# Kernel optimization log

Hardware: AMD Instinct MI355X
Metric: run time of the kernel (lower is better)

## Reference

```python
import jax, jax.numpy as jnp
import numpy as np

N, E, D, H, O, G = 50000, 640000, 128, 128, 16, 64


def setup_inputs() -> dict:
    key = jax.random.key(0)
    ks = jax.random.split(key, 10)
    x = jax.random.normal(ks[0], (N, D), dtype=jnp.float32)
    edge_index = jax.random.randint(ks[1], (2, E), 0, N, dtype=jnp.int64)
    edge_weight = jax.random.uniform(ks[2], (E,), dtype=jnp.float32)
    batch = jnp.sort(jax.random.randint(ks[3], (N,), 0, G, dtype=jnp.int64))
    s1 = 1.0 / np.sqrt(D)
    s2 = 1.0 / np.sqrt(H)
    W1 = jax.random.uniform(ks[4], (D, H), jnp.float32, -s1, s1)
    b1 = jnp.zeros((H,), jnp.float32)
    W2 = jax.random.uniform(ks[5], (H, H), jnp.float32, -s2, s2)
    b2 = jnp.zeros((H,), jnp.float32)
    Wfc = jax.random.uniform(ks[6], (H, O), jnp.float32, -s2, s2)
    bfc = jax.random.uniform(ks[7], (O,), jnp.float32, -s2, s2)
    return dict(x=x, edge_index=edge_index, edge_weight=edge_weight, batch=batch,
                W1=W1, b1=b1, W2=W2, b2=b2, Wfc=Wfc, bfc=bfc)


def _gcn_conv(x, row, col, ew, W, b, n):
    # PyG GCNConv: out[i] = sum_{(j->i)} norm_ji * (x[j] @ W) + b
    xw = x @ W
    deg = jax.ops.segment_sum(ew, col, num_segments=n)          # [N]
    dinv = jnp.where(deg > 0, jax.lax.rsqrt(deg), 0.0)
    norm = dinv[row] * ew * dinv[col]                           # [E+N]
    msg = xw[row] * norm[:, None]                               # gather + scale
    return jax.ops.segment_sum(msg, col, num_segments=n) + b    # scatter-add


def reference(x, edge_index, edge_weight, batch, W1, b1, W2, b2, Wfc, bfc):
    n = x.shape[0]
    # add self-loops with weight 1 (PyG gcn_norm default)
    loop = jnp.arange(n, dtype=edge_index.dtype)
    row = jnp.concatenate([edge_index[0], loop])
    col = jnp.concatenate([edge_index[1], loop])
    ew = jnp.concatenate([edge_weight, jnp.ones((n,), edge_weight.dtype)])

    h = jax.nn.relu(_gcn_conv(x, row, col, ew, W1, b1, n))
    h = jax.nn.relu(_gcn_conv(h, row, col, ew, W2, b2, n))

    # global_mean_pool over graph ids
    sums = jax.ops.segment_sum(h, batch, num_segments=G)        # [G, H]
    cnt = jax.ops.segment_sum(jnp.ones((n,), h.dtype), batch, num_segments=G)
    pooled = sums / jnp.maximum(cnt, 1.0)[:, None]
    return pooled @ Wfc + bfc                                   # [G, O]
```

## Files before the change

kernel.cpp:

```cpp
#include <hip/hip_runtime.h>


typedef _Float16 h4 __attribute__((ext_vector_type(4)));
typedef _Float16 h8 __attribute__((ext_vector_type(8)));
typedef float f32x4 __attribute__((ext_vector_type(4)));

__global__ void initcnt_kernel(int* __restrict__ cnt, int NC) {
    int i = blockIdx.x * blockDim.x + threadIdx.x;
    if (i < NC) cnt[i] = 0;
}

__global__ void rank_kernel(const int* __restrict__ row, const int* __restrict__ col,
                            int* __restrict__ cnt, int* __restrict__ rank, int E, int C) {
    int e = blockIdx.x * blockDim.x + threadIdx.x;
    if (e >= E) return;
    int key = col[e] * C + (row[e] >> 13);
    rank[e] = atomicAdd(&cnt[key], 1);
}

__global__ void block_sum_kernel(const int* __restrict__ cnt, int* __restrict__ bsum, int NC) {
    __shared__ int s[512];
    int t = threadIdx.x;
    int i = blockIdx.x * 512 + t;
    s[t] = (i < NC) ? cnt[i] : 0;
    __syncthreads();
    for (int off = 256; off > 0; off >>= 1) {
        if (t < off) s[t] += s[t + off];
        __syncthreads();
    }
    if (t == 0) bsum[blockIdx.x] = s[0];
}

__global__ void scan_bsum_kernel(const int* __restrict__ bsum, int* __restrict__ boff,
                                 int* __restrict__ rowptr, int NC, int nb) {
    __shared__ int s[1024];
    int t = threadIdx.x;
    int v = (t < nb) ? bsum[t] : 0;
    s[t] = v;
    __syncthreads();
    for (int off = 1; off < 1024; off <<= 1) {
        int u = (t >= off) ? s[t - off] : 0;
        __syncthreads();
        s[t] += u;
        __syncthreads();
    }
    if (t < nb) boff[t] = s[t] - v;
    if (t == nb - 1) rowptr[NC] = s[t];
}

__global__ void rowptr_kernel(const int* __restrict__ cnt, const int* __restrict__ boff,
                              int* __restrict__ rowptr, int NC) {
    __shared__ int s[512];
    int t = threadIdx.x;
    int i = blockIdx.x * 512 + t;
    int v = (i < NC) ? cnt[i] : 0;
    s[t] = v;
    __syncthreads();
    for (int off = 1; off < 512; off <<= 1) {
        int u = (t >= off) ? s[t - off] : 0;
        __syncthreads();
        s[t] += u;
        __syncthreads();
    }
    if (i < NC) rowptr[i] = boff[blockIdx.x] + s[t] - v;
}

__global__ void scatter_kernel(const int* __restrict__ row, const int* __restrict__ col,
                               const float* __restrict__ ew, const int* __restrict__ rank,
                               const int* __restrict__ rowptr, int2* __restrict__ csr,
                               int E, int C) {
    int e = blockIdx.x * blockDim.x + threadIdx.x;
    if (e >= E) return;
    int r = row[e];
    int pos = rowptr[col[e] * C + (r >> 13)] + rank[e];
    int2 v;
    v.x = r;
    v.y = __float_as_int(ew[e]);
    csr[pos] = v;
}

__global__ __launch_bounds__(256) void deginv_convert_kernel(
        const float4* __restrict__ x4, const int2* __restrict__ csr,
        const int* __restrict__ rowptr, float* __restrict__ dinv,
        h4* __restrict__ p16, int n, int C) {
    int node = blockIdx.x * 8 + (threadIdx.x >> 5);
    if (node >= n) return;
    int lane = threadIdx.x & 31;
    int beg = rowptr[node * C], end = rowptr[node * C + C];
    float sum = 0.0f;
    for (int k = beg + lane; k < end; k += 32) sum += __int_as_float(csr[k].y);
#pragma unroll
    for (int m = 16; m >= 1; m >>= 1) sum += __shfl_xor(sum, m);
    float di = rsqrtf(1.0f + sum);
    if (lane == 0) dinv[node] = di;
    float4 v = x4[(size_t)node * 32 + lane];
    h4 h;
    h.x = (_Float16)(di * v.x); h.y = (_Float16)(di * v.y);
    h.z = (_Float16)(di * v.z); h.w = (_Float16)(di * v.w);
    p16[(size_t)node * 32 + lane] = h;
}

__global__ __launch_bounds__(256) void agg_kernel(const h4* __restrict__ in16,
                                                  const int* __restrict__ rowptr,
                                                  const int2* __restrict__ csr,
                                                  const float* __restrict__ dinv,
                                                  h4* __restrict__ out16, int n, int C) {
    int node = blockIdx.x * 8 + (threadIdx.x >> 5);
    if (node >= n) return;
    int lane = threadIdx.x & 31;
    float di = dinv[node];
    h4 v = in16[(size_t)node * 32 + lane];
    float ax = (float)v.x, ay = (float)v.y, az = (float)v.z, aw = (float)v.w;
    int beg = rowptr[node * C], end = rowptr[node * C + C];
    int idx = beg;
    for (; idx + 4 <= end; idx += 4) {
        int2 e0 = csr[idx + 0], e1 = csr[idx + 1], e2 = csr[idx + 2], e3 = csr[idx + 3];
        h4 u0 = in16[(size_t)e0.x * 32 + lane];
        h4 u1 = in16[(size_t)e1.x * 32 + lane];
        h4 u2 = in16[(size_t)e2.x * 32 + lane];
        h4 u3 = in16[(size_t)e3.x * 32 + lane];
        float w0 = __int_as_float(e0.y), w1 = __int_as_float(e1.y);
        float w2 = __int_as_float(e2.y), w3 = __int_as_float(e3.y);
        ax += w0 * (float)u0.x; ay += w0 * (float)u0.y; az += w0 * (float)u0.z; aw += w0 * (float)u0.w;
        ax += w1 * (float)u1.x; ay += w1 * (float)u1.y; az += w1 * (float)u1.z; aw += w1 * (float)u1.w;
        ax += w2 * (float)u2.x; ay += w2 * (float)u2.y; az += w2 * (float)u2.z; aw += w2 * (float)u2.w;
        ax += w3 * (float)u3.x; ay += w3 * (float)u3.y; az += w3 * (float)u3.z; aw += w3 * (float)u3.w;
    }
    for (; idx < end; ++idx) {
        int2 e0 = csr[idx];
        float ww = __int_as_float(e0.y);
        h4 u = in16[(size_t)e0.x * 32 + lane];
        ax += ww * (float)u.x; ay += ww * (float)u.y;
        az += ww * (float)u.z; aw += ww * (float)u.w;
    }
    h4 r;
    r.x = (_Float16)(ax * di); r.y = (_Float16)(ay * di);
    r.z = (_Float16)(az * di); r.w = (_Float16)(aw * di);
    out16[(size_t)node * 32 + lane] = r;
}

__global__ __launch_bounds__(256) void packW_kernel(const float* __restrict__ W1,
                                                    const float* __restrict__ W2,
                                                    _Float16* __restrict__ Wp1,
                                                    _Float16* __restrict__ Wp2) {
    const float* W = blockIdx.x ? W2 : W1;
    _Float16* Wp = blockIdx.x ? Wp2 : Wp1;
    for (int i = threadIdx.x; i < 2048; i += 256) {
        int lane = i & 63, kc = i >> 6;
        int c = kc >> 2, kb = kc & 3;
        int colq = lane & 15, quad = lane >> 4;
        h8 v;
#pragma unroll
        for (int j = 0; j < 8; ++j)
            v[j] = (_Float16)W[(kb * 32 + quad * 8 + j) * 128 + c * 16 + colq];
        ((h8*)Wp)[i] = v;
    }
}

template <int SCALE>
__global__ __launch_bounds__(256) void gemm_mfma(const _Float16* __restrict__ A,
                                                 const h8* __restrict__ Wp,
                                                 const float* __restrict__ bias,
                                                 const float* __restrict__ dinv,
                                                 _Float16* __restrict__ out16, int n) {
    int wid = threadIdx.x >> 6, lane = threadIdx.x & 63;
    int tb = blockIdx.x * 64 + wid * 16;
    if (tb >= n) return;
    int colq = lane & 15, quad = lane >> 4;

    int arow = tb + colq;
    if (arow >= n) arow = n - 1;
    const h8* Arow = (const h8*)(A + (size_t)arow * 128);
    h8 a[4];
#pragma unroll
    for (int kb = 0; kb < 4; ++kb) a[kb] = Arow[kb * 4 + quad];

    f32x4 acc[8];
#pragma unroll
    for (int c = 0; c < 8; ++c) acc[c] = (f32x4)(0.0f);

#pragma unroll
    for (int c = 0; c < 8; ++c) {
#pragma unroll
        for (int kb = 0; kb < 4; ++kb) {
            h8 b = Wp[(c * 4 + kb) * 64 + lane];
            acc[c] = __builtin_amdgcn_mfma_f32_16x16x32_f16(a[kb], b, acc[c], 0, 0, 0);
        }
    }

#pragma unroll
    for (int c = 0; c < 8; ++c) {
        float bz = bias[c * 16 + colq];
#pragma unroll
        for (int r = 0; r < 4; ++r) {
            int row = tb + quad * 4 + r;
            if (row < n) {
                float v = fmaxf(acc[c][r] + bz, 0.0f);
                if (SCALE) v *= dinv[row];
                out16[(size_t)row * 128 + c * 16 + colq] = (_Float16)v;
            }
        }
    }
}

__global__ __launch_bounds__(256) void poolfc_kernel(const h4* __restrict__ h,
                                                     const int* __restrict__ batch,
                                                     const float* __restrict__ Wfc,
                                                     const float* __restrict__ bfc,
                                                     float* __restrict__ out, int n, int O) {
    int g = blockIdx.x;
    __shared__ int sb[2];
    __shared__ float4 red[256];
    __shared__ float pooled[128];
    int t = threadIdx.x;
    if (t < 2) {
        int target = g + t;
        int lo = 0, hi = n;
        while (lo < hi) { int m = (lo + hi) >> 1; if (batch[m] < target) lo = m + 1; else hi = m; }
        sb[t] = lo;
    }
    __syncthreads();
    int start = sb[0], end = sb[1], len = end - start;
    int gq = t & 31;
    int seg = t >> 5;
    float4 acc; acc.x = acc.y = acc.z = acc.w = 0.0f;
    for (int i = start + seg; i < end; i += 8) {
        h4 v = h[(size_t)i * 32 + gq];
        acc.x += (float)v.x; acc.y += (float)v.y;
        acc.z += (float)v.z; acc.w += (float)v.w;
    }
    red[seg * 32 + gq] = acc;
    __syncthreads();
    if (t < 128) {
        float4 a = red[t], b = red[t + 128];
        a.x += b.x; a.y += b.y; a.z += b.z; a.w += b.w;
        red[t] = a;
    }
    __syncthreads();
    if (t < 64) {
        float4 a = red[t], b = red[t + 64];
        a.x += b.x; a.y += b.y; a.z += b.z; a.w += b.w;
        red[t] = a;
    }
    __syncthreads();
    if (t < 32) {
        float4 a = red[t], b = red[t + 32];
        float inv = (len > 0) ? 1.0f / (float)len : 0.0f;
        pooled[t * 4 + 0] = (a.x + b.x) * inv;
        pooled[t * 4 + 1] = (a.y + b.y) * inv;
        pooled[t * 4 + 2] = (a.z + b.z) * inv;
        pooled[t * 4 + 3] = (a.w + b.w) * inv;
    }
    __syncthreads();
    if (t < O) {
        float a = bfc[t];
        for (int k = 0; k < 128; ++k) a += pooled[k] * Wfc[k * O + t];
        out[g * O + t] = a;
    }
}

extern "C" void kernel_launch(void* const* d_in, const int* in_sizes, int n_in,
                              void* d_out, int out_size, void* d_ws, size_t ws_size,
                              hipStream_t stream) {
    const float* x     = (const float*)d_in[0];
    const int*   ei    = (const int*)d_in[1];
    const float* ew    = (const float*)d_in[2];
    const int*   batch = (const int*)d_in[3];
    const float* W1    = (const float*)d_in[4];
    const float* b1    = (const float*)d_in[5];
    const float* W2    = (const float*)d_in[6];
    const float* b2    = (const float*)d_in[7];
    const float* Wfc   = (const float*)d_in[8];
    const float* bfc   = (const float*)d_in[9];
    float* out = (float*)d_out;

    const int n = in_sizes[0] / 128;
    const int E = in_sizes[2];
    const int O = in_sizes[9];
    const int G = out_size / O;
    const int* row = ei;
    const int* col = ei + E;
    const int C  = (n + 8191) >> 13;
    const int NC = n * C;
    const int NB = (NC + 511) / 512;

    char* p = (char*)d_ws;
    auto alloc = [&](size_t bytes) {
        char* r = p;
        p += (bytes + 255) & ~(size_t)255;
        return r;
    };
    float* dinv    = (float*)alloc((size_t)n * 4);
    int*   cnt     = (int*)alloc((size_t)NC * 4);
    int*   rank    = (int*)alloc((size_t)E * 4);
    int*   rowptr  = (int*)alloc((size_t)(NC + 1) * 4);
    int*   bsum    = (int*)alloc((size_t)NB * 4);
    int*   boff    = (int*)alloc((size_t)NB * 4);
    int2*  csr     = (int2*)alloc((size_t)E * 8);
    h4*    p1      = (h4*)alloc((size_t)n * 128 * 2);
    h4*    agg16   = (h4*)alloc((size_t)n * 128 * 2);
    h4*    p2      = (h4*)alloc((size_t)n * 128 * 2);
    h4*    h2      = (h4*)alloc((size_t)n * 128 * 2);
    _Float16* Wp1  = (_Float16*)alloc(128 * 128 * 2);
    _Float16* Wp2  = (_Float16*)alloc(128 * 128 * 2);

    initcnt_kernel<<<(NC + 255) / 256, 256, 0, stream>>>(cnt, NC);
    packW_kernel<<<2, 256, 0, stream>>>(W1, W2, Wp1, Wp2);
    rank_kernel<<<(E + 255) / 256, 256, 0, stream>>>(row, col, cnt, rank, E, C);
    block_sum_kernel<<<NB, 512, 0, stream>>>(cnt, bsum, NC);
    scan_bsum_kernel<<<1, 1024, 0, stream>>>(bsum, boff, rowptr, NC, NB);
    rowptr_kernel<<<NB, 512, 0, stream>>>(cnt, boff, rowptr, NC);
    scatter_kernel<<<(E + 255) / 256, 256, 0, stream>>>(row, col, ew, rank, rowptr, csr, E, C);
    deginv_convert_kernel<<<(n + 7) / 8, 256, 0, stream>>>((const float4*)x, csr, rowptr, dinv, p1, n, C);

    agg_kernel<<<(n + 7) / 8, 256, 0, stream>>>(p1, rowptr, csr, dinv, agg16, n, C);
    gemm_mfma<1><<<(n + 63) / 64, 256, 0, stream>>>((const _Float16*)agg16, (const h8*)Wp1,
                                                    b1, dinv, (_Float16*)p2, n);

    agg_kernel<<<(n + 7) / 8, 256, 0, stream>>>(p2, rowptr, csr, dinv, agg16, n, C);
    gemm_mfma<0><<<(n + 63) / 64, 256, 0, stream>>>((const _Float16*)agg16, (const h8*)Wp2,
                                                    b2, dinv, (_Float16*)h2, n);

    poolfc_kernel<<<G, 256, 0, stream>>>(h2, batch, Wfc, bfc, out, n, O);
}
```

Before: 265.0 us.

## Pack CSR edges into 32-bit words and shrink rank to 16 bits

Each CSR edge entry changes from an int2 (row, fp32 weight) to one 32-bit word: the source row sits in the upper 16 bits and the fp16 edge weight in the lower 16. Per-edge ranks are stored as unsigned short. This halves the edge-list traffic in the degree and aggregation kernels, whose CSR reads also become nontemporal loads. The counter-zeroing kernel is replaced by hipMemsetAsync. In exchange it assumes fewer than 65536 nodes and per-bucket counts below 65536, and it rounds edge weights to fp16.

```diff
diff --git a/kernel.cpp b/kernel.cpp
--- a/kernel.cpp
+++ b/kernel.cpp
@@ -5,17 +5,13 @@
 typedef _Float16 h8 __attribute__((ext_vector_type(8)));
 typedef float f32x4 __attribute__((ext_vector_type(4)));
 
-__global__ void initcnt_kernel(int* __restrict__ cnt, int NC) {
-    int i = blockIdx.x * blockDim.x + threadIdx.x;
-    if (i < NC) cnt[i] = 0;
-}
-
 __global__ void rank_kernel(const int* __restrict__ row, const int* __restrict__ col,
-                            int* __restrict__ cnt, int* __restrict__ rank, int E, int C) {
+                            int* __restrict__ cnt, unsigned short* __restrict__ rank,
+                            int E, int C) {
     int e = blockIdx.x * blockDim.x + threadIdx.x;
     if (e >= E) return;
     int key = col[e] * C + (row[e] >> 13);
-    rank[e] = atomicAdd(&cnt[key], 1);
+    rank[e] = (unsigned short)atomicAdd(&cnt[key], 1);
 }
 
 __global__ void block_sum_kernel(const int* __restrict__ cnt, int* __restrict__ bsum, int NC) {
@@ -66,21 +62,20 @@
 }
 
 __global__ void scatter_kernel(const int* __restrict__ row, const int* __restrict__ col,
-                               const float* __restrict__ ew, const int* __restrict__ rank,
-                               const int* __restrict__ rowptr, int2* __restrict__ csr,
-                               int E, int C) {
+                               const float* __restrict__ ew,
+                               const unsigned short* __restrict__ rank,
+                               const int* __restrict__ rowptr,
+                               unsigned int* __restrict__ csr, int E, int C) {
     int e = blockIdx.x * blockDim.x + threadIdx.x;
     if (e >= E) return;
     int r = row[e];
-    int pos = rowptr[col[e] * C + (r >> 13)] + rank[e];
-    int2 v;
-    v.x = r;
-    v.y = __float_as_int(ew[e]);
-    csr[pos] = v;
+    int pos = rowptr[col[e] * C + (r >> 13)] + (int)rank[e];
+    unsigned short hw = __builtin_bit_cast(unsigned short, (_Float16)ew[e]);
+    csr[pos] = ((unsigned int)r << 16) | (unsigned int)hw;
 }
 
 __global__ __launch_bounds__(256) void deginv_convert_kernel(
-        const float4* __restrict__ x4, const int2* __restrict__ csr,
+        const float4* __restrict__ x4, const unsigned int* __restrict__ csr,
         const int* __restrict__ rowptr, float* __restrict__ dinv,
         h4* __restrict__ p16, int n, int C) {
     int node = blockIdx.x * 8 + (threadIdx.x >> 5);
@@ -88,7 +83,10 @@
     int lane = threadIdx.x & 31;
     int beg = rowptr[node * C], end = rowptr[node * C + C];
     float sum = 0.0f;
-    for (int k = beg + lane; k < end; k += 32) sum += __int_as_float(csr[k].y);
+    for (int k = beg + lane; k < end; k += 32) {
+        unsigned int v = __builtin_nontemporal_load(csr + k);
+        sum += (float)__builtin_bit_cast(_Float16, (unsigned short)(v & 0xffffu));
+    }
 #pragma unroll
     for (int m = 16; m >= 1; m >>= 1) sum += __shfl_xor(sum, m);
     float di = rsqrtf(1.0f + sum);
@@ -102,7 +100,7 @@
 
 __global__ __launch_bounds__(256) void agg_kernel(const h4* __restrict__ in16,
                                                   const int* __restrict__ rowptr,
-                                                  const int2* __restrict__ csr,
+                                                  const unsigned int* __restrict__ csr,
                                                   const float* __restrict__ dinv,
                                                   h4* __restrict__ out16, int n, int C) {
     int node = blockIdx.x * 8 + (threadIdx.x >> 5);
@@ -114,22 +112,27 @@
     int beg = rowptr[node * C], end = rowptr[node * C + C];
     int idx = beg;
     for (; idx + 4 <= end; idx += 4) {
-        int2 e0 = csr[idx + 0], e1 = csr[idx + 1], e2 = csr[idx + 2], e3 = csr[idx + 3];
-        h4 u0 = in16[(size_t)e0.x * 32 + lane];
-        h4 u1 = in16[(size_t)e1.x * 32 + lane];
-        h4 u2 = in16[(size_t)e2.x * 32 + lane];
-        h4 u3 = in16[(size_t)e3.x * 32 + lane];
-        float w0 = __int_as_float(e0.y), w1 = __int_as_float(e1.y);
-        float w2 = __int_as_float(e2.y), w3 = __int_as_float(e3.y);
+        unsigned int e0 = __builtin_nontemporal_load(csr + idx + 0);
+        unsigned int e1 = __builtin_nontemporal_load(csr + idx + 1);
+        unsigned int e2 = __builtin_nontemporal_load(csr + idx + 2);
+        unsigned int e3 = __builtin_nontemporal_load(csr + idx + 3);
+        h4 u0 = in16[(size_t)(e0 >> 16) * 32 + lane];
+        h4 u1 = in16[(size_t)(e1 >> 16) * 32 + lane];
+        h4 u2 = in16[(size_t)(e2 >> 16) * 32 + lane];
+        h4 u3 = in16[(size_t)(e3 >> 16) * 32 + lane];
+        float w0 = (float)__builtin_bit_cast(_Float16, (unsigned short)(e0 & 0xffffu));
+        float w1 = (float)__builtin_bit_cast(_Float16, (unsigned short)(e1 & 0xffffu));
+        float w2 = (float)__builtin_bit_cast(_Float16, (unsigned short)(e2 & 0xffffu));
+        float w3 = (float)__builtin_bit_cast(_Float16, (unsigned short)(e3 & 0xffffu));
         ax += w0 * (float)u0.x; ay += w0 * (float)u0.y; az += w0 * (float)u0.z; aw += w0 * (float)u0.w;
         ax += w1 * (float)u1.x; ay += w1 * (float)u1.y; az += w1 * (float)u1.z; aw += w1 * (float)u1.w;
         ax += w2 * (float)u2.x; ay += w2 * (float)u2.y; az += w2 * (float)u2.z; aw += w2 * (float)u2.w;
         ax += w3 * (float)u3.x; ay += w3 * (float)u3.y; az += w3 * (float)u3.z; aw += w3 * (float)u3.w;
     }
     for (; idx < end; ++idx) {
-        int2 e0 = csr[idx];
-        float ww = __int_as_float(e0.y);
-        h4 u = in16[(size_t)e0.x * 32 + lane];
+        unsigned int e0 = __builtin_nontemporal_load(csr + idx);
+        float ww = (float)__builtin_bit_cast(_Float16, (unsigned short)(e0 & 0xffffu));
+        h4 u = in16[(size_t)(e0 >> 16) * 32 + lane];
         ax += ww * (float)u.x; ay += ww * (float)u.y;
         az += ww * (float)u.z; aw += ww * (float)u.w;
     }
@@ -292,11 +295,11 @@
     };
     float* dinv    = (float*)alloc((size_t)n * 4);
     int*   cnt     = (int*)alloc((size_t)NC * 4);
-    int*   rank    = (int*)alloc((size_t)E * 4);
+    unsigned short* rank = (unsigned short*)alloc((size_t)E * 2);
     int*   rowptr  = (int*)alloc((size_t)(NC + 1) * 4);
     int*   bsum    = (int*)alloc((size_t)NB * 4);
     int*   boff    = (int*)alloc((size_t)NB * 4);
-    int2*  csr     = (int2*)alloc((size_t)E * 8);
+    unsigned int* csr = (unsigned int*)alloc((size_t)E * 4);
     h4*    p1      = (h4*)alloc((size_t)n * 128 * 2);
     h4*    agg16   = (h4*)alloc((size_t)n * 128 * 2);
     h4*    p2      = (h4*)alloc((size_t)n * 128 * 2);
@@ -304,7 +307,7 @@
     _Float16* Wp1  = (_Float16*)alloc(128 * 128 * 2);
     _Float16* Wp2  = (_Float16*)alloc(128 * 128 * 2);
 
-    initcnt_kernel<<<(NC + 255) / 256, 256, 0, stream>>>(cnt, NC);
+    hipMemsetAsync(cnt, 0, (size_t)NC * 4, stream);
     packW_kernel<<<2, 256, 0, stream>>>(W1, W2, Wp1, Wp2);
     rank_kernel<<<(E + 255) / 256, 256, 0, stream>>>(row, col, cnt, rank, E, C);
     block_sum_kernel<<<NB, 512, 0, stream>>>(cnt, bsum, NC);
```

After: 267.7 us. Within noise of the previous version (+1.0%).
